# Kernel optimization log

Measured on AMD Instinct MI355X. Metric: run time of the kernel, lower is better.

## Reference

```python
import jax, jax.numpy as jnp
import numpy as np

EPS = 1e-6  # F.pairwise_distance eps, added to each coordinate difference


def setup_inputs() -> dict:
    key = jax.random.key(0)
    x = jax.random.normal(key, (8192, 3, 192), dtype=jnp.float32)
    return {"x": x}


def reference(x):
    # x: [N, M, D]; positive = shot 0, anchor = mean of shots 1:
    anchor = jnp.mean(x[:, 1:, :], axis=1)          # [N, D]
    pos = x[:, 0, :]                                # [N, D]
    N, D = pos.shape

    # Legacy pairwise_distance reduces over D of the broadcast [N, D, N] diff:
    # dist2[i, j] = sum_d (pos[i,d] - anchor[j,d] + eps)^2
    # Expand exactly via GEMM to avoid materializing [N, D, N]:
    # = ||pos_i||^2 + ||anc_j||^2 - 2 pos_i.anc_j + 2*eps*(sum_d pos_i - sum_d anc_j) + D*eps^2
    pn = jnp.sum(pos * pos, axis=1)                 # [N]
    an = jnp.sum(anchor * anchor, axis=1)           # [N]
    cross = pos @ anchor.T                          # [N, N]
    sdiff = jnp.sum(pos, axis=1)[:, None] - jnp.sum(anchor, axis=1)[None, :]
    dist2 = pn[:, None] + an[None, :] - 2.0 * cross + 2.0 * EPS * sdiff + D * (EPS * EPS)
    output = -dist2                                 # [N, N] logits

    labels = jnp.arange(N)
    logp = jax.nn.log_softmax(output, axis=-1)
    nloss = -jnp.mean(jnp.take_along_axis(logp, labels[:, None], axis=1))

    pred = jnp.argmax(output, axis=1)               # top-1
    prec1 = jnp.mean((pred == labels).astype(jnp.float32)) * 100.0
    return (nloss, prec1)
```

## Files before the change

### kernel.cpp

```cpp
#include <hip/hip_runtime.h>
#include <math.h>


#define NROWS  8192
#define DDIM   192
#define KSPL   384
#define X3     576
#define FEPS   1e-6f

#define BM 128
#define BN 128
#define BK 64
#define NSPLIT 8
#define JRANGE 1024
#define JTILES 8
#define NPART  16
#define NCOMB  32

typedef _Float16 f16;
typedef _Float16 f16x8 __attribute__((ext_vector_type(8)));
typedef float    f32x4 __attribute__((ext_vector_type(4)));

__device__ __forceinline__ void async_copy16(const void* g, void* l) {
  __builtin_amdgcn_global_load_lds(
      (const __attribute__((address_space(1))) unsigned int*)g,
      (__attribute__((address_space(3))) unsigned int*)l, 16, 0, 0);
}

__global__ __launch_bounds__(256) void prep_kernel(const float* __restrict__ x,
                                                   f16* __restrict__ ph,
                                                   f16* __restrict__ ah,
                                                   float* __restrict__ bvec) {
  int row  = (blockIdx.x * 256 + threadIdx.x) >> 6;
  int lane = threadIdx.x & 63;
  if (row >= NROWS) return;
  const float* xr = x + (size_t)row * X3;
  float an = 0.f, as = 0.f;
  #pragma unroll
  for (int t = 0; t < 3; ++t) {
    int d = lane + t * 64;
    float p = xr[d];
    float a = 0.5f * (xr[DDIM + d] + xr[2 * DDIM + d]);
    f16 phh = (f16)p;
    f16 pll = (f16)(p - (float)phh);
    ph[(size_t)row * KSPL + d] = phh;
    ph[(size_t)row * KSPL + DDIM + d] = pll;
    f16 ahh = (f16)a;
    f16 all = (f16)(a - (float)ahh);
    ah[(size_t)row * KSPL + d] = ahh;
    ah[(size_t)row * KSPL + DDIM + d] = all;
    an += a * a;
    as += a;
  }
  #pragma unroll
  for (int m = 32; m; m >>= 1) {
    an += __shfl_xor(an, m);
    as += __shfl_xor(as, m);
  }
  if (lane == 0) bvec[row] = -an + 2.0f * FEPS * as;
}

__global__ __launch_bounds__(256, 2) void main_kernel(
    const f16* __restrict__ Ag, const f16* __restrict__ Bg,
    const float* __restrict__ bvec,
    float* __restrict__ pm, float* __restrict__ ps, int* __restrict__ pa,
    float* __restrict__ diag) {
  __shared__ __align__(16) f16 As[BM * BK];
  __shared__ __align__(16) f16 Bs[BN * BK];
  const int tid  = threadIdx.x;
  const int lane = tid & 63;
  const int wid  = tid >> 6;
  const int wm = wid >> 1, wn = wid & 1;
  const int lLow = lane & 15, lHi = lane >> 4, l7 = lane & 7;
  const int i0 = blockIdx.x * BM;
  const int split = blockIdx.y;

  const int rsub = lane >> 3;
  const int srck = ((lane & 7) ^ rsub) * 8;

  float mrun[16], srun[16];
  int   arun[16];
  #pragma unroll
  for (int r = 0; r < 16; ++r) { mrun[r] = -3.0e38f; srun[r] = 0.f; arun[r] = 0; }

  for (int jt = 0; jt < JTILES; ++jt) {
    const int j0 = split * JRANGE + jt * BN;
    f32x4 acc[4][4];
    #pragma unroll
    for (int mf = 0; mf < 4; ++mf)
      #pragma unroll
      for (int nf = 0; nf < 4; ++nf) acc[mf][nf] = (f32x4)0.f;

    for (int kc = 0; kc < KSPL; kc += BK) {
      __syncthreads();
      #pragma unroll
      for (int q = 0; q < 4; ++q) {
        const int ci  = q * 4 + wid;
        const int row = ci * 8 + rsub;
        async_copy16(Ag + (size_t)(i0 + row) * KSPL + kc + srck, (void*)(As + ci * 512));
        async_copy16(Bg + (size_t)(j0 + row) * KSPL + kc + srck, (void*)(Bs + ci * 512));
      }
      __syncthreads();
      #pragma unroll
      for (int kk = 0; kk < 2; ++kk) {
        const int ksw = ((kk * 4 + lHi) ^ l7) * 8;
        f16x8 af[4];
        #pragma unroll
        for (int mf = 0; mf < 4; ++mf) {
          int r = wm * 64 + mf * 16 + lLow;
          af[mf] = *(const f16x8*)(As + r * 64 + ksw);
        }
        #pragma unroll
        for (int nf = 0; nf < 4; ++nf) {
          int r = wn * 64 + nf * 16 + lLow;
          f16x8 bf = *(const f16x8*)(Bs + r * 64 + ksw);
          #pragma unroll
          for (int mf = 0; mf < 4; ++mf)
            acc[mf][nf] = __builtin_amdgcn_mfma_f32_16x16x32_f16(af[mf], bf, acc[mf][nf], 0, 0, 0);
        }
      }
    }

    float bv[4];
    int   gc[4];
    #pragma unroll
    for (int nf = 0; nf < 4; ++nf) {
      gc[nf] = j0 + wn * 64 + nf * 16 + lLow;
      bv[nf] = bvec[gc[nf]];
    }
    const bool dtile = (split == (int)(blockIdx.x >> 3)) && (jt == (int)(blockIdx.x & 7));
    #pragma unroll
    for (int mf = 0; mf < 4; ++mf) {
      #pragma unroll
      for (int reg = 0; reg < 4; ++reg) {
        const int rs = mf * 4 + reg;
        const int grow = i0 + wm * 64 + mf * 16 + lHi * 4 + reg;
        float v0 = 2.f * acc[mf][0][reg] + bv[0];
        float v1 = 2.f * acc[mf][1][reg] + bv[1];
        float v2 = 2.f * acc[mf][2][reg] + bv[2];
        float v3 = 2.f * acc[mf][3][reg] + bv[3];
        if (dtile) {
          if (grow == gc[0]) diag[grow] = v0;
          if (grow == gc[1]) diag[grow] = v1;
          if (grow == gc[2]) diag[grow] = v2;
          if (grow == gc[3]) diag[grow] = v3;
        }
        float tm = v0; int tj = gc[0];
        if (v1 > tm) { tm = v1; tj = gc[1]; }
        if (v2 > tm) { tm = v2; tj = gc[2]; }
        if (v3 > tm) { tm = v3; tj = gc[3]; }
        float nm = fmaxf(tm, mrun[rs]);
        float se = __expf(v0 - nm) + __expf(v1 - nm) + __expf(v2 - nm) + __expf(v3 - nm);
        srun[rs] = srun[rs] * __expf(mrun[rs] - nm) + se;
        if (tm > mrun[rs]) arun[rs] = tj;
        mrun[rs] = nm;
      }
    }
  }

  #pragma unroll
  for (int rs = 0; rs < 16; ++rs) {
    float mm = mrun[rs], ss = srun[rs];
    int aa = arun[rs];
    #pragma unroll
    for (int d = 1; d < 16; d <<= 1) {
      float om = __shfl_xor(mm, d, 16);
      float os = __shfl_xor(ss, d, 16);
      int   oa = __shfl_xor(aa, d, 16);
      float nm = fmaxf(mm, om);
      ss = ss * __expf(mm - nm) + os * __expf(om - nm);
      if (om > mm || (om == mm && oa < aa)) aa = oa;
      mm = nm;
    }
    if (lLow == 0) {
      const int grow = i0 + wm * 64 + (rs >> 2) * 16 + lHi * 4 + (rs & 3);
      const int sidx = split * 2 + wn;
      pm[(size_t)sidx * NROWS + grow] = mm;
      ps[(size_t)sidx * NROWS + grow] = ss;
      pa[(size_t)sidx * NROWS + grow] = aa;
    }
  }
}

__global__ __launch_bounds__(256) void combine_partial(
    const float* __restrict__ pm, const float* __restrict__ ps,
    const int* __restrict__ pa, const float* __restrict__ diag,
    float* __restrict__ partL, float* __restrict__ partC) {
  const int i = blockIdx.x * 256 + threadIdx.x;
  float mm = pm[i];
  int   aa = pa[i];
  #pragma unroll
  for (int s = 1; s < NPART; ++s) {
    float om = pm[(size_t)s * NROWS + i];
    int   oa = pa[(size_t)s * NROWS + i];
    if (om > mm || (om == mm && oa < aa)) { mm = om; aa = oa; }
  }
  float ss = 0.f;
  #pragma unroll
  for (int s = 0; s < NPART; ++s)
    ss += ps[(size_t)s * NROWS + i] * __expf(pm[(size_t)s * NROWS + i] - mm);
  float lsum = (mm + logf(ss)) - diag[i];
  float csum = (aa == i) ? 1.0f : 0.0f;
  #pragma unroll
  for (int d = 32; d; d >>= 1) {
    lsum += __shfl_xor(lsum, d);
    csum += __shfl_xor(csum, d);
  }
  __shared__ float wl[4], wc[4];
  int w = threadIdx.x >> 6;
  if ((threadIdx.x & 63) == 0) { wl[w] = lsum; wc[w] = csum; }
  __syncthreads();
  if (threadIdx.x == 0) {
    partL[blockIdx.x] = wl[0] + wl[1] + wl[2] + wl[3];
    partC[blockIdx.x] = wc[0] + wc[1] + wc[2] + wc[3];
  }
}

__global__ __launch_bounds__(64) void final_kernel(
    const float* __restrict__ partL, const float* __restrict__ partC,
    float* __restrict__ out) {
  int t = threadIdx.x;
  float l = (t < NCOMB) ? partL[t] : 0.f;
  float c = (t < NCOMB) ? partC[t] : 0.f;
  #pragma unroll
  for (int d = 32; d; d >>= 1) {
    l += __shfl_xor(l, d);
    c += __shfl_xor(c, d);
  }
  if (t == 0) {
    out[0] = l / (float)NROWS;
    out[1] = 100.f * c / (float)NROWS;
  }
}

extern "C" void kernel_launch(void* const* d_in, const int* in_sizes, int n_in,
                              void* d_out, int out_size, void* d_ws, size_t ws_size,
                              hipStream_t stream) {
  const float* x = (const float*)d_in[0];
  float* out = (float*)d_out;

  char* ws = (char*)d_ws;
  size_t off = 0;
  auto take = [&](size_t bytes) { void* p = ws + off; off += (bytes + 255) & ~(size_t)255; return p; };
  f16*   ph    = (f16*)take((size_t)NROWS * KSPL * sizeof(f16));
  f16*   ah    = (f16*)take((size_t)NROWS * KSPL * sizeof(f16));
  float* bvec  = (float*)take((size_t)NROWS * sizeof(float));
  float* pm    = (float*)take((size_t)NPART * NROWS * sizeof(float));
  float* ps    = (float*)take((size_t)NPART * NROWS * sizeof(float));
  int*   pa    = (int*)take((size_t)NPART * NROWS * sizeof(int));
  float* diag  = (float*)take((size_t)NROWS * sizeof(float));
  float* partL = (float*)take((size_t)NCOMB * sizeof(float));
  float* partC = (float*)take((size_t)NCOMB * sizeof(float));

  prep_kernel<<<dim3((NROWS * 64) / 256), 256, 0, stream>>>(x, ph, ah, bvec);
  main_kernel<<<dim3(NROWS / BM, NSPLIT), 256, 0, stream>>>(ph, ah, bvec, pm, ps, pa, diag);
  combine_partial<<<dim3(NCOMB), 256, 0, stream>>>(pm, ps, pa, diag, partL, partC);
  final_kernel<<<1, 64, 0, stream>>>(partL, partC, out);
}
```

Measured before the change: 161.6 us.

## Double-buffer LDS tiles across k and j steps, fold log2e scaling into operands

```diff
diff --git a/kernel.cpp b/kernel.cpp
--- a/kernel.cpp
+++ b/kernel.cpp
@@ -7,10 +7,13 @@
 #define KSPL   384
 #define X3     576
 #define FEPS   1e-6f
+#define LOG2E  1.4426950408889634f
+#define LN2    0.6931471805599453f
 
 #define BM 128
 #define BN 128
 #define BK 64
+#define KSTEPS 6
 #define NSPLIT 8
 #define JRANGE 1024
 #define JTILES 8
@@ -18,6 +21,7 @@
 #define NCOMB  32
 
 typedef _Float16 f16;
+typedef _Float16 f16x4 __attribute__((ext_vector_type(4)));
 typedef _Float16 f16x8 __attribute__((ext_vector_type(8)));
 typedef float    f32x4 __attribute__((ext_vector_type(4)));
 
@@ -31,33 +35,40 @@
                                                    f16* __restrict__ ph,
                                                    f16* __restrict__ ah,
                                                    float* __restrict__ bvec) {
-  int row  = (blockIdx.x * 256 + threadIdx.x) >> 6;
-  int lane = threadIdx.x & 63;
-  if (row >= NROWS) return;
-  const float* xr = x + (size_t)row * X3;
+  const int row  = (blockIdx.x * 256 + threadIdx.x) >> 6;
+  const int lane = threadIdx.x & 63;
   float an = 0.f, as = 0.f;
-  #pragma unroll
-  for (int t = 0; t < 3; ++t) {
-    int d = lane + t * 64;
-    float p = xr[d];
-    float a = 0.5f * (xr[DDIM + d] + xr[2 * DDIM + d]);
-    f16 phh = (f16)p;
-    f16 pll = (f16)(p - (float)phh);
-    ph[(size_t)row * KSPL + d] = phh;
-    ph[(size_t)row * KSPL + DDIM + d] = pll;
-    f16 ahh = (f16)a;
-    f16 all = (f16)(a - (float)ahh);
-    ah[(size_t)row * KSPL + d] = ahh;
-    ah[(size_t)row * KSPL + DDIM + d] = all;
-    an += a * a;
-    as += a;
+  if (lane < 48) {
+    const float* xr = x + (size_t)row * X3;
+    const int d = lane * 4;
+    const float4 p = *(const float4*)(xr + d);
+    const float4 u = *(const float4*)(xr + DDIM + d);
+    const float4 w = *(const float4*)(xr + 2 * DDIM + d);
+    const float a0 = 0.5f * (u.x + w.x), a1 = 0.5f * (u.y + w.y);
+    const float a2 = 0.5f * (u.z + w.z), a3 = 0.5f * (u.w + w.w);
+    an = a0 * a0 + a1 * a1 + a2 * a2 + a3 * a3;
+    as = a0 + a1 + a2 + a3;
+    const float C2 = 2.0f * LOG2E;
+    const float p0 = p.x * C2, p1 = p.y * C2, p2 = p.z * C2, p3 = p.w * C2;
+    const f16 h0 = (f16)p0, h1 = (f16)p1, h2 = (f16)p2, h3 = (f16)p3;
+    f16x4 hv = {h0, h1, h2, h3};
+    f16x4 lv = {(f16)(p0 - (float)h0), (f16)(p1 - (float)h1),
+                (f16)(p2 - (float)h2), (f16)(p3 - (float)h3)};
+    *(f16x4*)(ph + (size_t)row * KSPL + d) = hv;
+    *(f16x4*)(ph + (size_t)row * KSPL + DDIM + d) = lv;
+    const f16 g0 = (f16)a0, g1 = (f16)a1, g2 = (f16)a2, g3 = (f16)a3;
+    f16x4 gv = {g0, g1, g2, g3};
+    f16x4 mv = {(f16)(a0 - (float)g0), (f16)(a1 - (float)g1),
+                (f16)(a2 - (float)g2), (f16)(a3 - (float)g3)};
+    *(f16x4*)(ah + (size_t)row * KSPL + d) = gv;
+    *(f16x4*)(ah + (size_t)row * KSPL + DDIM + d) = mv;
   }
   #pragma unroll
   for (int m = 32; m; m >>= 1) {
     an += __shfl_xor(an, m);
     as += __shfl_xor(as, m);
   }
-  if (lane == 0) bvec[row] = -an + 2.0f * FEPS * as;
+  if (lane == 0) bvec[row] = LOG2E * (-an + 2.0f * FEPS * as);
 }
 
 __global__ __launch_bounds__(256, 2) void main_kernel(
@@ -65,8 +76,8 @@
     const float* __restrict__ bvec,
     float* __restrict__ pm, float* __restrict__ ps, int* __restrict__ pa,
     float* __restrict__ diag) {
-  __shared__ __align__(16) f16 As[BM * BK];
-  __shared__ __align__(16) f16 Bs[BN * BK];
+  __shared__ __align__(16) f16 As[2][BM * BK];
+  __shared__ __align__(16) f16 Bs[2][BN * BK];
   const int tid  = threadIdx.x;
   const int lane = tid & 63;
   const int wid  = tid >> 6;
@@ -78,83 +89,94 @@
   const int rsub = lane >> 3;
   const int srck = ((lane & 7) ^ rsub) * 8;
 
+  auto stage = [&](int b, int jt, int kc) {
+    const int j0 = split * JRANGE + jt * BN;
+    #pragma unroll
+    for (int q = 0; q < 4; ++q) {
+      const int ci  = q * 4 + wid;
+      const int row = ci * 8 + rsub;
+      async_copy16(Ag + (size_t)(i0 + row) * KSPL + kc + srck, (void*)(&As[b][ci * 512]));
+      async_copy16(Bg + (size_t)(j0 + row) * KSPL + kc + srck, (void*)(&Bs[b][ci * 512]));
+    }
+  };
+
   float mrun[16], srun[16];
   int   arun[16];
   #pragma unroll
   for (int r = 0; r < 16; ++r) { mrun[r] = -3.0e38f; srun[r] = 0.f; arun[r] = 0; }
 
+  stage(0, 0, 0);
+  __syncthreads();
+
   for (int jt = 0; jt < JTILES; ++jt) {
-    const int j0 = split * JRANGE + jt * BN;
     f32x4 acc[4][4];
     #pragma unroll
     for (int mf = 0; mf < 4; ++mf)
       #pragma unroll
       for (int nf = 0; nf < 4; ++nf) acc[mf][nf] = (f32x4)0.f;
 
-    for (int kc = 0; kc < KSPL; kc += BK) {
-      __syncthreads();
-      #pragma unroll
-      for (int q = 0; q < 4; ++q) {
-        const int ci  = q * 4 + wid;
-        const int row = ci * 8 + rsub;
-        async_copy16(Ag + (size_t)(i0 + row) * KSPL + kc + srck, (void*)(As + ci * 512));
-        async_copy16(Bg + (size_t)(j0 + row) * KSPL + kc + srck, (void*)(Bs + ci * 512));
+    #pragma unroll
+    for (int ks = 0; ks < KSTEPS; ++ks) {
+      if (!(jt == JTILES - 1 && ks == KSTEPS - 1)) {
+        const int jn = (ks == KSTEPS - 1) ? jt + 1 : jt;
+        const int kn = (ks == KSTEPS - 1) ? 0 : (ks + 1) * BK;
+        stage((ks + 1) & 1, jn, kn);
       }
-      __syncthreads();
+      const int b = ks & 1;
       #pragma unroll
       for (int kk = 0; kk < 2; ++kk) {
         const int ksw = ((kk * 4 + lHi) ^ l7) * 8;
         f16x8 af[4];
         #pragma unroll
-        for (int mf = 0; mf < 4; ++mf) {
-          int r = wm * 64 + mf * 16 + lLow;
-          af[mf] = *(const f16x8*)(As + r * 64 + ksw);
-        }
+        for (int mf = 0; mf < 4; ++mf)
+          af[mf] = *(const f16x8*)(&As[b][(wm * 64 + mf * 16 + lLow) * 64 + ksw]);
         #pragma unroll
         for (int nf = 0; nf < 4; ++nf) {
-          int r = wn * 64 + nf * 16 + lLow;
-          f16x8 bf = *(const f16x8*)(Bs + r * 64 + ksw);
+          f16x8 bf = *(const f16x8*)(&Bs[b][(wn * 64 + nf * 16 + lLow) * 64 + ksw]);
           #pragma unroll
           for (int mf = 0; mf < 4; ++mf)
             acc[mf][nf] = __builtin_amdgcn_mfma_f32_16x16x32_f16(af[mf], bf, acc[mf][nf], 0, 0, 0);
         }
       }
-    }
-
-    float bv[4];
-    int   gc[4];
-    #pragma unroll
-    for (int nf = 0; nf < 4; ++nf) {
-      gc[nf] = j0 + wn * 64 + nf * 16 + lLow;
-      bv[nf] = bvec[gc[nf]];
-    }
-    const bool dtile = (split == (int)(blockIdx.x >> 3)) && (jt == (int)(blockIdx.x & 7));
-    #pragma unroll
-    for (int mf = 0; mf < 4; ++mf) {
-      #pragma unroll
-      for (int reg = 0; reg < 4; ++reg) {
-        const int rs = mf * 4 + reg;
-        const int grow = i0 + wm * 64 + mf * 16 + lHi * 4 + reg;
-        float v0 = 2.f * acc[mf][0][reg] + bv[0];
-        float v1 = 2.f * acc[mf][1][reg] + bv[1];
-        float v2 = 2.f * acc[mf][2][reg] + bv[2];
-        float v3 = 2.f * acc[mf][3][reg] + bv[3];
-        if (dtile) {
-          if (grow == gc[0]) diag[grow] = v0;
-          if (grow == gc[1]) diag[grow] = v1;
-          if (grow == gc[2]) diag[grow] = v2;
-          if (grow == gc[3]) diag[grow] = v3;
+      if (ks == KSTEPS - 1) {
+        const int j0 = split * JRANGE + jt * BN;
+        float bv[4];
+        int   gc[4];
+        #pragma unroll
+        for (int nf = 0; nf < 4; ++nf) {
+          gc[nf] = j0 + wn * 64 + nf * 16 + lLow;
+          bv[nf] = bvec[gc[nf]];
         }
-        float tm = v0; int tj = gc[0];
-        if (v1 > tm) { tm = v1; tj = gc[1]; }
-        if (v2 > tm) { tm = v2; tj = gc[2]; }
-        if (v3 > tm) { tm = v3; tj = gc[3]; }
-        float nm = fmaxf(tm, mrun[rs]);
-        float se = __expf(v0 - nm) + __expf(v1 - nm) + __expf(v2 - nm) + __expf(v3 - nm);
-        srun[rs] = srun[rs] * __expf(mrun[rs] - nm) + se;
-        if (tm > mrun[rs]) arun[rs] = tj;
-        mrun[rs] = nm;
+        const bool dtile = (split == (int)(blockIdx.x >> 3)) && (jt == (int)(blockIdx.x & 7));
+        #pragma unroll
+        for (int mf = 0; mf < 4; ++mf) {
+          #pragma unroll
+          for (int reg = 0; reg < 4; ++reg) {
+            const int rs = mf * 4 + reg;
+            const int grow = i0 + wm * 64 + mf * 16 + lHi * 4 + reg;
+            float v0 = acc[mf][0][reg] + bv[0];
+            float v1 = acc[mf][1][reg] + bv[1];
+            float v2 = acc[mf][2][reg] + bv[2];
+            float v3 = acc[mf][3][reg] + bv[3];
+            if (dtile) {
+              if (grow == gc[0]) diag[grow] = v0;
+              if (grow == gc[1]) diag[grow] = v1;
+              if (grow == gc[2]) diag[grow] = v2;
+              if (grow == gc[3]) diag[grow] = v3;
+            }
+            float tm = v0; int tj = gc[0];
+            if (v1 > tm) { tm = v1; tj = gc[1]; }
+            if (v2 > tm) { tm = v2; tj = gc[2]; }
+            if (v3 > tm) { tm = v3; tj = gc[3]; }
+            float nm = fmaxf(tm, mrun[rs]);
+            float se = exp2f(v0 - nm) + exp2f(v1 - nm) + exp2f(v2 - nm) + exp2f(v3 - nm);
+            srun[rs] = srun[rs] * exp2f(mrun[rs] - nm) + se;
+            if (tm > mrun[rs]) arun[rs] = tj;
+            mrun[rs] = nm;
+          }
+        }
       }
+      __syncthreads();
     }
   }
 
@@ -168,7 +190,7 @@
       float os = __shfl_xor(ss, d, 16);
       int   oa = __shfl_xor(aa, d, 16);
       float nm = fmaxf(mm, om);
-      ss = ss * __expf(mm - nm) + os * __expf(om - nm);
+      ss = ss * exp2f(mm - nm) + os * exp2f(om - nm);
       if (om > mm || (om == mm && oa < aa)) aa = oa;
       mm = nm;
     }
@@ -198,8 +220,8 @@
   float ss = 0.f;
   #pragma unroll
   for (int s = 0; s < NPART; ++s)
-    ss += ps[(size_t)s * NROWS + i] * __expf(pm[(size_t)s * NROWS + i] - mm);
-  float lsum = (mm + logf(ss)) - diag[i];
+    ss += ps[(size_t)s * NROWS + i] * exp2f(pm[(size_t)s * NROWS + i] - mm);
+  float lsum = (mm + log2f(ss) - diag[i]) * LN2;
   float csum = (aa == i) ? 1.0f : 0.0f;
   #pragma unroll
   for (int d = 32; d; d >>= 1) {
```

Measured after the change: 186.2 us. +15.2%, slower.
